# Kernel tuning notes

Hardware: AMD Instinct MI355X
Metric: run time of the kernel (lower is better)

## Reference

```python
import jax, jax.numpy as jnp
import numpy as np
from jax import lax

B, T, D, FF, E, TOPK, CLS = 16, 512, 1024, 2048, 4, 2, 1200
KW = 3  # conv kernel width per ff_kernelsize=[3,3]


def _sinusoidal_pe(T, D):
    pos = np.arange(T, dtype=np.float32)[:, None]
    div = np.exp(np.arange(0, D, 2, dtype=np.float32) * (-np.log(10000.0) / D))
    pe = np.zeros((T, D), dtype=np.float32)
    pe[:, 0::2] = np.sin(pos * div)
    pe[:, 1::2] = np.cos(pos * div)
    return jnp.asarray(pe)


def setup_inputs() -> dict:
    key = jax.random.key(0)
    ks = jax.random.split(key, 12)
    sc = 0.02
    x = jax.random.normal(ks[0], (B, T, D), jnp.float32)
    mask = jax.random.randint(ks[1], (B, T), 0, 2).astype(jnp.int32)
    mask = mask.at[:, 0].set(1)  # ensure >=1 valid token
    return {
        "x": x,
        "mask": mask,
        "fc1_w": jax.random.normal(ks[2], (D, D), jnp.float32) * sc,
        "fc1_b": jnp.zeros((D,), jnp.float32),
        "bn_g": jnp.ones((D,), jnp.float32),
        "bn_b": jnp.zeros((D,), jnp.float32),
        "pe": _sinusoidal_pe(T, D),
        "gate_w": jax.random.normal(ks[3], (D, E), jnp.float32) * sc,
        "ew1": jax.random.normal(ks[4], (E, FF, D, KW), jnp.float32) * sc,  # OIH per expert
        "eb1": jnp.zeros((E, FF), jnp.float32),
        "ew2": jax.random.normal(ks[5], (E, D, FF, KW), jnp.float32) * sc,
        "eb2": jnp.zeros((E, D), jnp.float32),
        "ln_g": jnp.ones((D,), jnp.float32),
        "ln_b": jnp.zeros((D,), jnp.float32),
        "out_w": jax.random.normal(ks[6], (CLS, D), jnp.float32) * sc,
        "out_b": jnp.zeros((CLS,), jnp.float32),
    }


def _forward(x, mask, fc1_w, fc1_b, bn_g, bn_b, pe, gate_w, ew1, eb1, ew2, eb2, ln_g, ln_b, out_w, out_b):
    mf = mask.astype(x.dtype)[..., None]  # [B,T,1]

    # fc1
    h = jnp.einsum("btd,ed->bte", x, fc1_w) + fc1_b

    # MaskedNorm (batch): stats over valid tokens only, invalid positions passed through
    cnt = jnp.maximum(jnp.sum(mf), 1.0)
    mean = jnp.sum(h * mf, axis=(0, 1)) / cnt
    var = jnp.sum(mf * (h - mean) ** 2, axis=(0, 1)) / cnt
    normed = (h - mean) * lax.rsqrt(var + 1e-5) * bn_g + bn_b
    h = jnp.where(mf > 0, normed, h)

    # ReLU + positional encoding (+ dropout is identity in eval)
    h = jax.nn.relu(h) + pe[None, :, :]

    # --- MoE with top-2 gating over 4 conv-FFN experts ---
    logits_g = jnp.einsum("btd,de->bte", h, gate_w)  # [B,T,E]
    probs_g = jax.nn.softmax(logits_g, axis=-1)
    top_v, top_i = lax.top_k(logits_g, TOPK)  # [B,T,K]
    top_g = jax.nn.softmax(top_v, axis=-1)
    # scatter top-k gates into dense [B,T,E] (E=4, cheap)
    gates = jnp.sum(top_g[..., None] * jax.nn.one_hot(top_i, E, dtype=h.dtype), axis=2)

    ht = jnp.transpose(h, (0, 2, 1))  # [B,D,T] for NCH conv

    def expert(w1, b1, w2, b2):
        y = lax.conv_general_dilated(ht, w1, (1,), "SAME", dimension_numbers=("NCH", "OIH", "NCH"))
        y = jax.nn.relu(y + b1[None, :, None])
        y = lax.conv_general_dilated(y, w2, (1,), "SAME", dimension_numbers=("NCH", "OIH", "NCH"))
        return y + b2[None, :, None]  # [B,D,T]

    ys = jax.vmap(expert)(ew1, eb1, ew2, eb2)  # [E,B,D,T]
    moe_out = jnp.einsum("bte,ebdt->btd", gates, ys)

    # load-balancing aux loss (Switch-style)
    frac = jnp.mean((gates > 0).astype(h.dtype), axis=(0, 1))  # tokens per expert
    imp = jnp.mean(probs_g, axis=(0, 1))
    aux_loss = E * jnp.sum(frac * imp)

    # LayerNorm (eps 1e-6)
    mu = jnp.mean(moe_out, axis=-1, keepdims=True)
    v = jnp.mean((moe_out - mu) ** 2, axis=-1, keepdims=True)
    feat = (moe_out - mu) * lax.rsqrt(v + 1e-6) * ln_g + ln_b

    logits = jnp.einsum("btd,cd->btc", feat, out_w) + out_b
    logp = jax.nn.log_softmax(logits, axis=2)
    p = jnp.exp(logp)
    feat_norm = feat / jnp.maximum(jnp.linalg.norm(feat, axis=-1, keepdims=True), 1e-12)
    return feat, feat_norm, logits, logp, p, aux_loss


def reference(x, mask, fc1_w, fc1_b, bn_g, bn_b, pe, gate_w, ew1, eb1, ew2, eb2, ln_g, ln_b, out_w, out_b):
    return _forward(x, mask, fc1_w, fc1_b, bn_g, bn_b, pe, gate_w, ew1, eb1, ew2, eb2, ln_g, ln_b, out_w, out_b)
```

## Files before the change

kernel.cpp:

```cpp
#include <hip/hip_runtime.h>
#include <hip/hip_bf16.h>


namespace {

constexpr int kB = 16, kT = 512, kD = 1024, kFF = 2048, kE = 4, kCLS = 1200;
constexpr int kM = kB * kT;
constexpr int kTP = kT + 2;
constexpr int kCLSP = 1280;
constexpr size_t kBTD = (size_t)kM * kD;
constexpr size_t kBTC = (size_t)kM * kCLS;
constexpr size_t kY1S = (size_t)kB * kTP * kFF;
constexpr size_t kTapStride = (size_t)kFF * kD;

constexpr size_t WS_H     = 0;
constexpr size_t WS_HPAD  = WS_H + kBTD;
constexpr size_t WS_Y1P   = WS_HPAD + (size_t)kB * kTP * kD / 2;
constexpr size_t WS_W1T   = WS_Y1P + (size_t)kB * kTP * kFF / 2;
constexpr size_t WS_W2T   = WS_W1T + (size_t)3 * kFF * kD / 2;
constexpr size_t WS_GATES = WS_W2T + (size_t)3 * kD * kFF / 2;
constexpr size_t WS_PROBS = WS_GATES + (size_t)kM * kE;
constexpr size_t WS_W1HI  = WS_PROBS + (size_t)kM * kE;
constexpr size_t WS_W1LO  = WS_W1HI + (size_t)kD * kD / 2;
constexpr size_t WS_OWB   = WS_W1LO + (size_t)kD * kD / 2;
constexpr size_t WS_SUMS  = WS_OWB + (size_t)kCLSP * kD / 2;
constexpr size_t WS_SUMSQ = WS_SUMS + kD;
constexpr size_t WS_CNT   = WS_SUMSQ + kD;
constexpr size_t WS_AA    = WS_CNT + 1;
constexpr size_t WS_CC    = WS_AA + kD;
constexpr int WS_ZERON = (int)(2 * kD + 1);

constexpr size_t BW_H     = 0;
constexpr size_t BW_HPAD  = BW_H + kBTD;
constexpr size_t BW_Y1    = BW_HPAD + (size_t)kB * kTP * kD / 2;
constexpr size_t BW_W1T   = BW_Y1 + (size_t)kE * kY1S / 2;
constexpr size_t BW_W2T   = BW_W1T + (size_t)kE * 3 * kFF * kD / 2;
constexpr size_t BW_GATES = BW_W2T + (size_t)kE * 3 * kD * kFF / 2;
constexpr size_t BW_PROBS = BW_GATES + (size_t)kM * kE;
constexpr size_t BW_W1HI  = BW_PROBS + (size_t)kM * kE;
constexpr size_t BW_W1LO  = BW_W1HI + (size_t)kD * kD / 2;
constexpr size_t BW_OWB   = BW_W1LO + (size_t)kD * kD / 2;
constexpr size_t BW_SUMS  = BW_OWB + (size_t)kCLSP * kD / 2;
constexpr size_t BW_SUMSQ = BW_SUMS + kD;
constexpr size_t BW_CNT   = BW_SUMSQ + kD;
constexpr size_t BW_AA    = BW_CNT + 1;
constexpr size_t BW_CC    = BW_AA + kD;
constexpr size_t BW_END   = BW_CC + kD;

typedef __attribute__((ext_vector_type(8))) short short8;
typedef __attribute__((ext_vector_type(4))) float f32x4;

#define GLOBAL_LOAD_LDS16(gp, lp)                                          \
  __builtin_amdgcn_global_load_lds(                                        \
      (const __attribute__((address_space(1))) void*)(gp),                 \
      (__attribute__((address_space(3))) void*)(lp), 16, 0, 0)

__device__ __forceinline__ float block_reduce_sum(float v, float* red) {
  const int tid = threadIdx.x;
  __syncthreads();
  red[tid] = v;
  __syncthreads();
  for (int s = 128; s > 0; s >>= 1) {
    if (tid < s) red[tid] += red[tid + s];
    __syncthreads();
  }
  return red[0];
}

__device__ __forceinline__ float block_reduce_max(float v, float* red) {
  const int tid = threadIdx.x;
  __syncthreads();
  red[tid] = v;
  __syncthreads();
  for (int s = 128; s > 0; s >>= 1) {
    if (tid < s) red[tid] = fmaxf(red[tid], red[tid + s]);
    __syncthreads();
  }
  return red[0];
}

__global__ void k_zero(float* __restrict__ p, int n) {
  int i = blockIdx.x * 256 + threadIdx.x;
  if (i < n) p[i] = 0.f;
}

__global__ void k_zero_bnd(__hip_bfloat16* __restrict__ Hpad,
                           __hip_bfloat16* __restrict__ Y1pad) {
  const int b = blockIdx.x >> 1;
  const int row = b * kTP + ((blockIdx.x & 1) ? (kTP - 1) : 0);
  const __hip_bfloat16 z = __float2bfloat16(0.f);
  for (int d = threadIdx.x; d < kD; d += 256) Hpad[(size_t)row * kD + d] = z;
  for (int d = threadIdx.x; d < kFF; d += 256) Y1pad[(size_t)row * kFF + d] = z;
}

__global__ void k_zero_bnd_all(__hip_bfloat16* __restrict__ Hpad,
                               __hip_bfloat16* __restrict__ Y1all) {
  const int g = blockIdx.x;
  const int which = g / (2 * kB);
  const int r = g % (2 * kB);
  const int b = r >> 1;
  const int row = b * kTP + ((r & 1) ? (kTP - 1) : 0);
  const __hip_bfloat16 z = __float2bfloat16(0.f);
  if (which == 0) {
    for (int d = threadIdx.x; d < kD; d += 256) Hpad[(size_t)row * kD + d] = z;
  } else {
    __hip_bfloat16* Y = Y1all + (size_t)(which - 1) * kY1S;
    for (int d = threadIdx.x; d < kFF; d += 256) Y[(size_t)row * kFF + d] = z;
  }
}

__global__ __launch_bounds__(256) void k_split(const float* __restrict__ src,
                                               __hip_bfloat16* __restrict__ hi,
                                               __hip_bfloat16* __restrict__ lo,
                                               int n4) {
  const int i = blockIdx.x * 256 + threadIdx.x;
  if (i >= n4) return;
  const float4 v = *reinterpret_cast<const float4*>(src + (size_t)i * 4);
  const float vv[4] = {v.x, v.y, v.z, v.w};
  unsigned short h[4], l[4];
#pragma unroll
  for (int j = 0; j < 4; ++j) {
    __hip_bfloat16 hb = __float2bfloat16(vv[j]);
    __hip_bfloat16 lb = __float2bfloat16(vv[j] - __bfloat162float(hb));
    h[j] = *reinterpret_cast<unsigned short*>(&hb);
    l[j] = *reinterpret_cast<unsigned short*>(&lb);
  }
  *reinterpret_cast<short4*>(hi + (size_t)i * 4) =
      make_short4(h[0], h[1], h[2], h[3]);
  *reinterpret_cast<short4*>(lo + (size_t)i * 4) =
      make_short4(l[0], l[1], l[2], l[3]);
}

__global__ __launch_bounds__(256) void k_wcast_pad(
    const float* __restrict__ w, __hip_bfloat16* __restrict__ dst) {
  const size_t i = (size_t)blockIdx.x * 256 + threadIdx.x;
  if (i >= (size_t)kCLSP * kD) return;
  const size_t r = i / kD;
  dst[i] = __float2bfloat16(r < kCLS ? w[i] : 0.f);
}

__global__ __launch_bounds__(256) void k_wt(const float* __restrict__ src,
                                            __hip_bfloat16* __restrict__ dst,
                                            int n) {
  const int i = blockIdx.x * 256 + threadIdx.x;
  if (i >= n) return;
  const float* s = src + (size_t)i * 3;
  dst[i] = __float2bfloat16(s[0]);
  dst[(size_t)n + i] = __float2bfloat16(s[1]);
  dst[(size_t)2 * n + i] = __float2bfloat16(s[2]);
}

__global__ __launch_bounds__(256) void k_wt_all(const float* __restrict__ ew1,
                                                const float* __restrict__ ew2,
                                                __hip_bfloat16* __restrict__ W1T,
                                                __hip_bfloat16* __restrict__ W2T) {
  const size_t n = (size_t)kFF * kD;
  const size_t total = (size_t)kE * n;
  const size_t i = (size_t)blockIdx.x * 256 + threadIdx.x;
  if (i >= total) return;
  const size_t e = i / n, j = i - e * n;
  {
    const float* s = ew1 + (e * n + j) * 3;
    __hip_bfloat16* d = W1T + e * 3 * n;
    d[j] = __float2bfloat16(s[0]);
    d[n + j] = __float2bfloat16(s[1]);
    d[2 * n + j] = __float2bfloat16(s[2]);
  }
  {
    const float* s = ew2 + (e * n + j) * 3;
    __hip_bfloat16* d = W2T + e * 3 * n;
    d[j] = __float2bfloat16(s[0]);
    d[n + j] = __float2bfloat16(s[1]);
    d[2 * n + j] = __float2bfloat16(s[2]);
  }
}

__global__ __launch_bounds__(256) void k_fc1_mfma(
    const __hip_bfloat16* __restrict__ Xhi, const __hip_bfloat16* __restrict__ Xlo,
    const __hip_bfloat16* __restrict__ Whi, const __hip_bfloat16* __restrict__ Wlo,
    const float* __restrict__ bias, float* __restrict__ H) {
  __shared__ __align__(16) __hip_bfloat16 As[128 * 32];
  __shared__ __align__(16) __hip_bfloat16 Bs[128 * 32];
  const int tid = threadIdx.x;
  const int m0 = blockIdx.y * 128;
  const int n0 = blockIdx.x * 128;
  const int w = tid >> 6, lane = tid & 63;
  const int wm = (w >> 1) * 64, wn = (w & 1) * 64;
  f32x4 acc[4][4] = {};
  const int fr = lane & 15, fc = (lane >> 4) * 8;
  const __hip_bfloat16* Aps[3] = {Xhi, Xlo, Xhi};
  const __hip_bfloat16* Bps[3] = {Whi, Whi, Wlo};
  for (int p = 0; p < 3; ++p) {
    const __hip_bfloat16* Ab = Aps[p] + (size_t)m0 * kD;
    const __hip_bfloat16* Bb = Bps[p] + (size_t)n0 * kD;
    for (int k0 = 0; k0 < kD; k0 += 32) {
      __syncthreads();
#pragma unroll
      for (int r = 0; r < 2; ++r) {
        const int idx = r * 256 + tid;
        const int row = idx >> 2, cg = (idx & 3) * 8;
        GLOBAL_LOAD_LDS16(Ab + (size_t)row * kD + k0 + cg, &As[idx * 8]);
        GLOBAL_LOAD_LDS16(Bb + (size_t)row * kD + k0 + cg, &Bs[idx * 8]);
      }
      __syncthreads();
      short8 af[4], bf[4];
#pragma unroll
      for (int i = 0; i < 4; ++i) {
        af[i] = *reinterpret_cast<const short8*>(&As[(wm + i * 16 + fr) * 32 + fc]);
        bf[i] = *reinterpret_cast<const short8*>(&Bs[(wn + i * 16 + fr) * 32 + fc]);
      }
#pragma unroll
      for (int i = 0; i < 4; ++i)
#pragma unroll
        for (int j = 0; j < 4; ++j)
          acc[i][j] = __builtin_amdgcn_mfma_f32_16x16x32_bf16(af[i], bf[j], acc[i][j], 0, 0, 0);
    }
  }
  const int cr = (lane >> 4) * 4, cc = lane & 15;
#pragma unroll
  for (int i = 0; i < 4; ++i) {
#pragma unroll
    for (int r = 0; r < 4; ++r) {
      const int m = m0 + wm + i * 16 + cr + r;
#pragma unroll
      for (int j = 0; j < 4; ++j) {
        const int gc = n0 + wn + j * 16 + cc;
        H[(size_t)m * kD + gc] = acc[i][j][r] + bias[gc];
      }
    }
  }
}

__global__ __launch_bounds__(256) void k_cls_mfma(
    const __hip_bfloat16* __restrict__ Fb, const __hip_bfloat16* __restrict__ Wb,
    const float* __restrict__ bias, float* __restrict__ logits) {
  __shared__ __align__(16) __hip_bfloat16 As[128 * 32];
  __shared__ __align__(16) __hip_bfloat16 Bs[128 * 32];
  const int tid = threadIdx.x;
  const int m0 = blockIdx.y * 128;
  const int n0 = blockIdx.x * 128;
  const int w = tid >> 6, lane = tid & 63;
  const int wm = (w >> 1) * 64, wn = (w & 1) * 64;
  f32x4 acc[4][4] = {};
  const int fr = lane & 15, fc = (lane >> 4) * 8;
  const __hip_bfloat16* Ab = Fb + (size_t)m0 * kD;
  const __hip_bfloat16* Bb = Wb + (size_t)n0 * kD;
  for (int k0 = 0; k0 < kD; k0 += 32) {
    __syncthreads();
#pragma unroll
    for (int r = 0; r < 2; ++r) {
      const int idx = r * 256 + tid;
      const int row = idx >> 2, cg = (idx & 3) * 8;
      GLOBAL_LOAD_LDS16(Ab + (size_t)row * kD + k0 + cg, &As[idx * 8]);
      GLOBAL_LOAD_LDS16(Bb + (size_t)row * kD + k0 + cg, &Bs[idx * 8]);
    }
    __syncthreads();
    short8 af[4], bf[4];
#pragma unroll
    for (int i = 0; i < 4; ++i) {
      af[i] = *reinterpret_cast<const short8*>(&As[(wm + i * 16 + fr) * 32 + fc]);
      bf[i] = *reinterpret_cast<const short8*>(&Bs[(wn + i * 16 + fr) * 32 + fc]);
    }
#pragma unroll
    for (int i = 0; i < 4; ++i)
#pragma unroll
      for (int j = 0; j < 4; ++j)
        acc[i][j] = __builtin_amdgcn_mfma_f32_16x16x32_bf16(af[i], bf[j], acc[i][j], 0, 0, 0);
  }
  const int cr = (lane >> 4) * 4, cc = lane & 15;
#pragma unroll
  for (int i = 0; i < 4; ++i) {
#pragma unroll
    for (int r = 0; r < 4; ++r) {
      const int m = m0 + wm + i * 16 + cr + r;
#pragma unroll
      for (int j = 0; j < 4; ++j) {
        const int gc = n0 + wn + j * 16 + cc;
        if (gc < kCLS) logits[(size_t)m * kCLS + gc] = acc[i][j][r] + bias[gc];
      }
    }
  }
}

__global__ __launch_bounds__(256) void k_conv1_mfma(
    const __hip_bfloat16* __restrict__ Hpad, const __hip_bfloat16* __restrict__ W1T,
    const float* __restrict__ b1, __hip_bfloat16* __restrict__ Y1pad) {
  __shared__ __align__(16) __hip_bfloat16 As[128 * 32];
  __shared__ __align__(16) __hip_bfloat16 Bs[128 * 32];
  const int tid = threadIdx.x;
  const int m0 = blockIdx.y * 128;
  const int n0 = blockIdx.x * 128;
  const int b = m0 >> 9;
  const int t0 = m0 & (kT - 1);
  const int arow0 = b * kTP + t0;
  const int w = tid >> 6, lane = tid & 63;
  const int wm = (w >> 1) * 64, wn = (w & 1) * 64;
  f32x4 acc[4][4] = {};
  const int fr = lane & 15, fc = (lane >> 4) * 8;
  for (int kk = 0; kk < 3; ++kk) {
    const __hip_bfloat16* Ab = Hpad + (size_t)(arow0 + kk) * kD;
    const __hip_bfloat16* Bb = W1T + (size_t)kk * kFF * kD + (size_t)n0 * kD;
    for (int k0 = 0; k0 < kD; k0 += 32) {
      __syncthreads();
#pragma unroll
      for (int r = 0; r < 2; ++r) {
        const int idx = r * 256 + tid;
        const int row = idx >> 2, cg = (idx & 3) * 8;
        GLOBAL_LOAD_LDS16(Ab + (size_t)row * kD + k0 + cg, &As[idx * 8]);
        GLOBAL_LOAD_LDS16(Bb + (size_t)row * kD + k0 + cg, &Bs[idx * 8]);
      }
      __syncthreads();
      short8 af[4], bf[4];
#pragma unroll
      for (int i = 0; i < 4; ++i) {
        af[i] = *reinterpret_cast<const short8*>(&As[(wm + i * 16 + fr) * 32 + fc]);
        bf[i] = *reinterpret_cast<const short8*>(&Bs[(wn + i * 16 + fr) * 32 + fc]);
      }
#pragma unroll
      for (int i = 0; i < 4; ++i)
#pragma unroll
        for (int j = 0; j < 4; ++j)
          acc[i][j] = __builtin_amdgcn_mfma_f32_16x16x32_bf16(af[i], bf[j], acc[i][j], 0, 0, 0);
    }
  }
  const int orow0 = b * kTP + t0 + 1;
  const int cr = (lane >> 4) * 4, cc = lane & 15;
#pragma unroll
  for (int i = 0; i < 4; ++i) {
#pragma unroll
    for (int r = 0; r < 4; ++r) {
      const int lr = wm + i * 16 + cr + r;
#pragma unroll
      for (int j = 0; j < 4; ++j) {
        const int gc = n0 + wn + j * 16 + cc;
        const float v = acc[i][j][r] + b1[gc];
        Y1pad[(size_t)(orow0 + lr) * kFF + gc] = __float2bfloat16(fmaxf(v, 0.f));
      }
    }
  }
}

__global__ __launch_bounds__(256) void k_conv2_mfma(
    const __hip_bfloat16* __restrict__ Y1pad, const __hip_bfloat16* __restrict__ W2T,
    const float* __restrict__ b2, const float* __restrict__ gates,
    int e, float* __restrict__ moe) {
  __shared__ __align__(16) __hip_bfloat16 As[128 * 32];
  __shared__ __align__(16) __hip_bfloat16 Bs[128 * 32];
  const int tid = threadIdx.x;
  const int m0 = blockIdx.y * 128;
  const int n0 = blockIdx.x * 128;
  const int b = m0 >> 9;
  const int t0 = m0 & (kT - 1);
  const int arow0 = b * kTP + t0;
  const int w = tid >> 6, lane = tid & 63;
  const int wm = (w >> 1) * 64, wn = (w & 1) * 64;
  f32x4 acc[4][4] = {};
  const int fr = lane & 15, fc = (lane >> 4) * 8;
  for (int kk = 0; kk < 3; ++kk) {
    const __hip_bfloat16* Ab = Y1pad + (size_t)(arow0 + kk) * kFF;
    const __hip_bfloat16* Bb = W2T + (size_t)kk * kD * kFF + (size_t)n0 * kFF;
    for (int k0 = 0; k0 < kFF; k0 += 32) {
      __syncthreads();
#pragma unroll
      for (int r = 0; r < 2; ++r) {
        const int idx = r * 256 + tid;
        const int row = idx >> 2, cg = (idx & 3) * 8;
        GLOBAL_LOAD_LDS16(Ab + (size_t)row * kFF + k0 + cg, &As[idx * 8]);
        GLOBAL_LOAD_LDS16(Bb + (size_t)row * kFF + k0 + cg, &Bs[idx * 8]);
      }
      __syncthreads();
      short8 af[4], bf[4];
#pragma unroll
      for (int i = 0; i < 4; ++i) {
        af[i] = *reinterpret_cast<const short8*>(&As[(wm + i * 16 + fr) * 32 + fc]);
        bf[i] = *reinterpret_cast<const short8*>(&Bs[(wn + i * 16 + fr) * 32 + fc]);
      }
#pragma unroll
      for (int i = 0; i < 4; ++i)
#pragma unroll
        for (int j = 0; j < 4; ++j)
          acc[i][j] = __builtin_amdgcn_mfma_f32_16x16x32_bf16(af[i], bf[j], acc[i][j], 0, 0, 0);
    }
  }
  const int cr = (lane >> 4) * 4, cc = lane & 15;
#pragma unroll
  for (int i = 0; i < 4; ++i) {
#pragma unroll
    for (int r = 0; r < 4; ++r) {
      const int lr = wm + i * 16 + cr + r;
      const int m = m0 + lr;
      const float g = gates[(size_t)m * kE + e];
#pragma unroll
      for (int j = 0; j < 4; ++j) {
        const int gc = n0 + wn + j * 16 + cc;
        const float v = acc[i][j][r] + b2[gc];
        const size_t idx = (size_t)m * kD + gc;
        moe[idx] = (e == 0 ? 0.f : moe[idx]) + g * v;
      }
    }
  }
}

#define WAITBAR(N)                                  \
  do {                                              \
    asm volatile("s_waitcnt vmcnt(" #N ")");        \
    __builtin_amdgcn_s_barrier();                   \
    __builtin_amdgcn_sched_barrier(0);              \
  } while (0)

#define QUAD(D, MH, NH, LOADA)                                                \
  do {                                                                        \
    const int _d = (D);                                                       \
    if (LOADA) {                                                              \
      const int _ab = ((_d * 2 + (MH)) << 14) + (fr << 6) + (fc << 1);        \
      _Pragma("unroll") for (int _i = 0; _i < 4; ++_i)                        \
          _Pragma("unroll") for (int _ks = 0; _ks < 2; ++_ks)                 \
              areg[_i][_ks] = *reinterpret_cast<const short8*>(               \
                  smem + ((_ab + (((wr * 4 + _i) * 2 + _ks) << 10)) ^ aswz)); \
    }                                                                         \
    short8 breg[2][2];                                                        \
    const int _bb =                                                           \
        65536 + ((_d * 2 + (NH)) << 14) + (fr << 6) + (fc << 1);              \
    _Pragma("unroll") for (int _j = 0; _j < 2; ++_j)                          \
        _Pragma("unroll") for (int _ks = 0; _ks < 2; ++_ks)                   \
            breg[_j][_ks] = *reinterpret_cast<const short8*>(                 \
                smem + ((_bb + (((wc * 2 + _j) * 2 + _ks) << 10)) ^ aswz));   \
    __builtin_amdgcn_s_setprio(1);                                            \
    _Pragma("unroll") for (int _i = 0; _i < 4; ++_i)                          \
        _Pragma("unroll") for (int _j = 0; _j < 2; ++_j)                      \
            _Pragma("unroll") for (int _ks = 0; _ks < 2; ++_ks)               \
                acc[MH][NH][_i][_j] =                                         \
                    __builtin_amdgcn_mfma_f32_16x16x32_bf16(                  \
                        areg[_i][_ks], breg[_j][_ks], acc[MH][NH][_i][_j],    \
                        0, 0, 0);                                             \
    __builtin_amdgcn_s_setprio(0);                                            \
  } while (0)

template <int K1, bool CONV1>
__global__ __launch_bounds__(512, 2) void k_conv8ph(
    const __hip_bfloat16* __restrict__ Asrc,
    const __hip_bfloat16* __restrict__ Wt,
    const float* __restrict__ bias,
    const float* __restrict__ gates,
    __hip_bfloat16* __restrict__ Yout,
    float* __restrict__ moe) {
  constexpr int NTOT = CONV1 ? kFF : kD;
  constexpr int NX = NTOT / 256;
  constexpr int NY = kM / 256;
  constexpr int NWG = kE * NY * NX;
  constexpr int KT1 = K1 / 64;
  constexpr int NT = 3 * KT1;
  extern __shared__ __align__(16) char smem[];

  int lid = blockIdx.x;
  lid = (lid & 7) * (NWG / 8) + (lid >> 3);
  const int e = lid / (NY * NX);
  const int rem = lid - e * (NY * NX);
  const int by = rem / NX, bx = rem - by * NX;
  const int m0 = by * 256, n0 = bx * 256;
  const int b = m0 >> 9, t0 = m0 & (kT - 1);
  const int arow0 = b * kTP + t0;

  const int tid = threadIdx.x;
  const int w = tid >> 6, l = tid & 63;
  const int wr = w >> 2, wc = w & 3;
  const int fr = l & 15, fc = (l >> 4) << 3;
  const int aswz = (fr & 8) ? 32 : 0;
  const int srr = l >> 2;
  const int scc = ((l & 3) << 3) ^ ((l & 32) ? 16 : 0);

  const __hip_bfloat16* Apan =
      (CONV1 ? Asrc : (Asrc + (size_t)e * kY1S)) + (size_t)arow0 * K1;
  const __hip_bfloat16* Bpan = Wt + (size_t)e * 3 * kTapStride + (size_t)n0 * K1;

  auto stageA = [&](int tau, int d, int mh) {
    const int kk = tau / KT1, kf = (tau % KT1) << 6;
    const __hip_bfloat16* org = Apan + (size_t)(kk + mh * 128) * K1 + kf;
    const int lb = (d * 2 + mh) << 14;
#pragma unroll
    for (int r = 0; r < 2; ++r) {
      const int s = w + r * 8;
      GLOBAL_LOAD_LDS16(org + (size_t)((s >> 1) * 16 + srr) * K1 +
                            ((s & 1) << 5) + scc,
                        smem + lb + (s << 10));
    }
  };
  auto stageB = [&](int tau, int d, int nh) {
    const int kk = tau / KT1, kf = (tau % KT1) << 6;
    const __hip_bfloat16* org =
        Bpan + (size_t)kk * kTapStride + (size_t)(nh * 128) * K1 + kf;
    const int lb = 65536 + ((d * 2 + nh) << 14);
#pragma unroll
    for (int r = 0; r < 2; ++r) {
      const int s = w + r * 8;
      GLOBAL_LOAD_LDS16(org + (size_t)((s >> 1) * 16 + srr) * K1 +
                            ((s & 1) << 5) + scc,
                        smem + lb + (s << 10));
    }
  };

  f32x4 acc[2][2][4][2] = {};
  short8 areg[4][2];

  stageA(0, 0, 0);
  stageB(0, 0, 0);
  stageB(0, 0, 1);
  stageA(0, 0, 1);

  for (int tau = 0; tau < NT - 1; ++tau) {
    const int d = tau & 1, dn = d ^ 1;
    WAITBAR(4); stageA(tau + 1, dn, 0); QUAD(d, 0, 0, true);
    WAITBAR(4); stageB(tau + 1, dn, 0); QUAD(d, 0, 1, false);
    WAITBAR(4); stageB(tau + 1, dn, 1); QUAD(d, 1, 0, true);
                stageA(tau + 1, dn, 1); QUAD(d, 1, 1, false);
  }
  {
    const int d = (NT - 1) & 1;
    WAITBAR(4); QUAD(d, 0, 0, true);
    WAITBAR(2); QUAD(d, 0, 1, false);
    WAITBAR(0); QUAD(d, 1, 0, true);
                QUAD(d, 1, 1, false);
  }

  const int cr = (l >> 4) * 4, cc = l & 15;
  if (CONV1) {
    __hip_bfloat16* Yb = Yout + (size_t)e * kY1S;
    const float* be = bias + (size_t)e * kFF;
    const int orow0 = b * kTP + t0 + 1;
#pragma unroll
    for (int mh = 0; mh < 2; ++mh)
#pragma unroll
      for (int i = 0; i < 4; ++i)
#pragma unroll
        for (int r = 0; r < 4; ++r) {
          const int rl = mh * 128 + wr * 64 + i * 16 + cr + r;
#pragma unroll
          for (int nh = 0; nh < 2; ++nh)
#pragma unroll
            for (int j = 0; j < 2; ++j) {
              const int gc = n0 + nh * 128 + wc * 32 + j * 16 + cc;
              const float v = acc[mh][nh][i][j][r] + be[gc];
              Yb[(size_t)(orow0 + rl) * kFF + gc] =
                  __float2bfloat16(fmaxf(v, 0.f));
            }
        }
  } else {
    const float* be = bias + (size_t)e * kD;
#pragma unroll
    for (int mh = 0; mh < 2; ++mh)
#pragma unroll
      for (int i = 0; i < 4; ++i)
#pragma unroll
        for (int r = 0; r < 4; ++r) {
          const int rl = mh * 128 + wr * 64 + i * 16 + cr + r;
          const int m = m0 + rl;
          const float g = gates[(size_t)m * kE + e];
#pragma unroll
          for (int nh = 0; nh < 2; ++nh)
#pragma unroll
            for (int j = 0; j < 2; ++j) {
              const int gc = n0 + nh * 128 + wc * 32 + j * 16 + cc;
              const float v = acc[mh][nh][i][j][r] + be[gc];
              atomicAdd(&moe[(size_t)m * kD + gc], g * v);
            }
        }
  }
}

__global__ __launch_bounds__(256) void k_cnt(const int* __restrict__ mask,
                                             float* __restrict__ cnt) {
  __shared__ float red[256];
  const int i = blockIdx.x * 256 + threadIdx.x;
  float v = (float)mask[i];
  v = block_reduce_sum(v, red);
  if (threadIdx.x == 0) atomicAdd(cnt, v);
}

__global__ __launch_bounds__(256) void k_stats(const float* __restrict__ H,
                                               const int* __restrict__ mask,
                                               float* __restrict__ sums,
                                               float* __restrict__ sumsq) {
  const int ch = blockIdx.x * 256 + threadIdx.x;
  const int r0 = blockIdx.y * 64;
  float s = 0.f, q = 0.f;
  for (int r = r0; r < r0 + 64; ++r) {
    if (mask[r]) {
      const float v = H[(size_t)r * kD + ch];
      s += v;
      q += v * v;
    }
  }
  atomicAdd(&sums[ch], s);
  atomicAdd(&sumsq[ch], q);
}

__global__ __launch_bounds__(256) void k_finalize(
    const float* __restrict__ sums, const float* __restrict__ sumsq,
    const float* __restrict__ cntp, const float* __restrict__ bn_g,
    const float* __restrict__ bn_b, float* __restrict__ aa,
    float* __restrict__ cc) {
  const int d = blockIdx.x * 256 + threadIdx.x;
  const float cnt = fmaxf(*cntp, 1.f);
  const float mean = sums[d] / cnt;
  const float var = sumsq[d] / cnt - mean * mean;
  const float istd = rsqrtf(var + 1e-5f);
  const float a = bn_g[d] * istd;
  aa[d] = a;
  cc[d] = bn_b[d] - mean * a;
}

__global__ __launch_bounds__(256) void k_norm_gate(
    const float* __restrict__ H, const int* __restrict__ mask,
    const float* __restrict__ pe, const float* __restrict__ aa,
    const float* __restrict__ cc, const float* __restrict__ gw,
    __hip_bfloat16* __restrict__ Hpad, float* __restrict__ gates,
    float* __restrict__ probs) {
  __shared__ float red[256];
  __shared__ float glog[4];
  const int r = blockIdx.x;
  const int tid = threadIdx.x;
  const int b = r >> 9;
  const int t = r & (kT - 1);
  const bool mv = mask[r] != 0;
  const size_t orow = (size_t)(b * kTP + t + 1) * kD;
  float gl[4] = {0.f, 0.f, 0.f, 0.f};
#pragma unroll
  for (int j = 0; j < 4; ++j) {
    const int d = tid + j * 256;
    float v = H[(size_t)r * kD + d];
    if (mv) v = v * aa[d] + cc[d];
    v = fmaxf(v, 0.f) + pe[(size_t)t * kD + d];
    Hpad[orow + d] = __float2bfloat16(v);
    const float4 g = *reinterpret_cast<const float4*>(gw + (size_t)d * 4);
    gl[0] += v * g.x; gl[1] += v * g.y; gl[2] += v * g.z; gl[3] += v * g.w;
  }
  for (int e = 0; e < 4; ++e) {
    const float s = block_reduce_sum(gl[e], red);
    if (tid == 0) glog[e] = s;
  }
  __syncthreads();
  if (tid == 0) {
    float lg[4] = {glog[0], glog[1], glog[2], glog[3]};
    const float mx = fmaxf(fmaxf(lg[0], lg[1]), fmaxf(lg[2], lg[3]));
    float ex[4], s = 0.f;
#pragma unroll
    for (int e = 0; e < 4; ++e) { ex[e] = expf(lg[e] - mx); s += ex[e]; }
    int i0 = 0;
    for (int e = 1; e < 4; ++e) if (lg[e] > lg[i0]) i0 = e;
    int i1 = -1;
    for (int e = 0; e < 4; ++e) {
      if (e == i0) continue;
      if (i1 < 0 || lg[e] > lg[i1]) i1 = e;
    }
    const float g0 = 1.f / (1.f + expf(lg[i1] - lg[i0]));
    float gv[4] = {0.f, 0.f, 0.f, 0.f};
    gv[i0] = g0;
    gv[i1] = 1.f - g0;
    *reinterpret_cast<float4*>(gates + (size_t)r * 4) =
        make_float4(gv[0], gv[1], gv[2], gv[3]);
    const float inv_s = 1.f / s;
    *reinterpret_cast<float4*>(probs + (size_t)r * 4) =
        make_float4(ex[0] * inv_s, ex[1] * inv_s, ex[2] * inv_s, ex[3] * inv_s);
  }
}

__global__ __launch_bounds__(256) void k_ln(
    const float* __restrict__ moe, const float* __restrict__ g,
    const float* __restrict__ b, float* __restrict__ feat,
    float* __restrict__ featn, __hip_bfloat16* __restrict__ featb) {
  __shared__ float red[256];
  const int r = blockIdx.x;
  const int tid = threadIdx.x;
  float v[4];
  float s = 0.f, q = 0.f;
#pragma unroll
  for (int j = 0; j < 4; ++j) {
    v[j] = moe[(size_t)r * kD + tid + j * 256];
    s += v[j];
    q += v[j] * v[j];
  }
  const float sum = block_reduce_sum(s, red);
  const float mu = sum * (1.f / kD);
  const float sq = block_reduce_sum(q, red);
  const float var = sq * (1.f / kD) - mu * mu;
  const float istd = rsqrtf(var + 1e-6f);
  float f[4];
  float fs = 0.f;
#pragma unroll
  for (int j = 0; j < 4; ++j) {
    const int d = tid + j * 256;
    f[j] = (v[j] - mu) * istd * g[d] + b[d];
    feat[(size_t)r * kD + d] = f[j];
    featb[(size_t)r * kD + d] = __float2bfloat16(f[j]);
    fs += f[j] * f[j];
  }
  const float nrm2 = block_reduce_sum(fs, red);
  const float scale = 1.f / fmaxf(sqrtf(nrm2), 1e-12f);
#pragma unroll
  for (int j = 0; j < 4; ++j) {
    const int d = tid + j * 256;
    featn[(size_t)r * kD + d] = f[j] * scale;
  }
}

__global__ __launch_bounds__(256) void k_softmax(
    const float* __restrict__ logits, float* __restrict__ logp,
    float* __restrict__ p) {
  __shared__ float red[256];
  const int r = blockIdx.x;
  const int tid = threadIdx.x;
  float lv[5];
  float mx = -1e30f;
#pragma unroll
  for (int j = 0; j < 5; ++j) {
    const int c = tid + j * 256;
    if (c < kCLS) {
      lv[j] = logits[(size_t)r * kCLS + c];
      mx = fmaxf(mx, lv[j]);
    }
  }
  mx = block_reduce_max(mx, red);
  float s = 0.f;
#pragma unroll
  for (int j = 0; j < 5; ++j) {
    const int c = tid + j * 256;
    if (c < kCLS) s += expf(lv[j] - mx);
  }
  s = block_reduce_sum(s, red);
  const float lse = mx + logf(s);
#pragma unroll
  for (int j = 0; j < 5; ++j) {
    const int c = tid + j * 256;
    if (c < kCLS) {
      const float lp = lv[j] - lse;
      logp[(size_t)r * kCLS + c] = lp;
      p[(size_t)r * kCLS + c] = expf(lp);
    }
  }
}

__global__ __launch_bounds__(256) void k_aux(const float* __restrict__ probs,
                                             const float* __restrict__ gates,
                                             float* __restrict__ out) {
  __shared__ float red[256];
  const int tid = threadIdx.x;
  float si[4] = {0.f, 0.f, 0.f, 0.f};
  float sf[4] = {0.f, 0.f, 0.f, 0.f};
  for (int i = tid; i < kM; i += 256) {
    const float4 p = *reinterpret_cast<const float4*>(probs + (size_t)i * 4);
    const float4 g = *reinterpret_cast<const float4*>(gates + (size_t)i * 4);
    si[0] += p.x; si[1] += p.y; si[2] += p.z; si[3] += p.w;
    sf[0] += (g.x > 0.f) ? 1.f : 0.f;
    sf[1] += (g.y > 0.f) ? 1.f : 0.f;
    sf[2] += (g.z > 0.f) ? 1.f : 0.f;
    sf[3] += (g.w > 0.f) ? 1.f : 0.f;
  }
  float tot = 0.f;
  for (int e = 0; e < 4; ++e) {
    const float S = block_reduce_sum(si[e], red);
    const float F = block_reduce_sum(sf[e], red);
    tot += (F / (float)kM) * (S / (float)kM);
  }
  if (tid == 0) out[0] = (float)kE * tot;
}

}

extern "C" void kernel_launch(void* const* d_in, const int* in_sizes, int n_in,
                              void* d_out, int out_size, void* d_ws,
                              size_t ws_size, hipStream_t stream) {
  const float* x     = (const float*)d_in[0];
  const int*   mask  = (const int*)d_in[1];
  const float* fc1_w = (const float*)d_in[2];
  const float* fc1_b = (const float*)d_in[3];
  const float* bn_g  = (const float*)d_in[4];
  const float* bn_b  = (const float*)d_in[5];
  const float* pe    = (const float*)d_in[6];
  const float* gw    = (const float*)d_in[7];
  const float* ew1   = (const float*)d_in[8];
  const float* eb1   = (const float*)d_in[9];
  const float* ew2   = (const float*)d_in[10];
  const float* eb2   = (const float*)d_in[11];
  const float* ln_g  = (const float*)d_in[12];
  const float* ln_b  = (const float*)d_in[13];
  const float* out_w = (const float*)d_in[14];
  const float* out_b = (const float*)d_in[15];

  float* ws = (float*)d_ws;

  float* outf   = (float*)d_out;
  float* feat   = outf;
  float* featn  = outf + kBTD;
  float* logits = outf + 2 * kBTD;
  float* logp   = logits + kBTC;
  float* pprob  = logp + kBTC;
  float* aux    = pprob + kBTC;

  const bool batched = ws_size >= BW_END * sizeof(float);

  if (batched) {
    float* H     = ws + BW_H;
    __hip_bfloat16* HPAD  = (__hip_bfloat16*)(ws + BW_HPAD);
    __hip_bfloat16* Y1ALL = (__hip_bfloat16*)(ws + BW_Y1);
    __hip_bfloat16* XHI   = Y1ALL;
    __hip_bfloat16* XLO   = XHI + kBTD;
    __hip_bfloat16* FEATB = Y1ALL;
    __hip_bfloat16* W1T   = (__hip_bfloat16*)(ws + BW_W1T);
    __hip_bfloat16* W2T   = (__hip_bfloat16*)(ws + BW_W2T);
    float* GATES = ws + BW_GATES;
    float* PROBS = ws + BW_PROBS;
    __hip_bfloat16* W1HI = (__hip_bfloat16*)(ws + BW_W1HI);
    __hip_bfloat16* W1LO = (__hip_bfloat16*)(ws + BW_W1LO);
    __hip_bfloat16* OWB  = (__hip_bfloat16*)(ws + BW_OWB);
    float* SUMS  = ws + BW_SUMS;
    float* MOE   = H;

    k_zero<<<dim3((WS_ZERON + 255) / 256), 256, 0, stream>>>(SUMS, WS_ZERON);
    k_split<<<dim3((int)(kBTD / 4 + 255) / 256), 256, 0, stream>>>(
        x, XHI, XLO, (int)(kBTD / 4));
    k_split<<<dim3((kD * kD / 4 + 255) / 256), 256, 0, stream>>>(
        fc1_w, W1HI, W1LO, kD * kD / 4);
    k_fc1_mfma<<<dim3(kD / 128, kM / 128), 256, 0, stream>>>(
        XHI, XLO, W1HI, W1LO, fc1_b, H);
    k_zero_bnd_all<<<dim3(2 * kB * (1 + kE)), 256, 0, stream>>>(HPAD, Y1ALL);
    k_wt_all<<<dim3((int)(((size_t)kE * kFF * kD + 255) / 256)), 256, 0,
               stream>>>(ew1, ew2, W1T, W2T);
    k_cnt<<<dim3(kM / 256), 256, 0, stream>>>(mask, ws + BW_CNT);
    k_stats<<<dim3(kD / 256, kM / 64), 256, 0, stream>>>(H, mask, SUMS,
                                                         ws + BW_SUMSQ);
    k_finalize<<<dim3(kD / 256), 256, 0, stream>>>(
        SUMS, ws + BW_SUMSQ, ws + BW_CNT, bn_g, bn_b, ws + BW_AA, ws + BW_CC);
    k_norm_gate<<<dim3(kM), 256, 0, stream>>>(H, mask, pe, ws + BW_AA,
                                              ws + BW_CC, gw, HPAD, GATES,
                                              PROBS);
    k_zero<<<dim3((int)((kBTD + 255) / 256)), 256, 0, stream>>>(MOE,
                                                                (int)kBTD);
    k_conv8ph<kD, true><<<dim3(kE * (kM / 256) * (kFF / 256)), 512, 131072,
                          stream>>>(HPAD, W1T, eb1, nullptr, Y1ALL, nullptr);
    k_conv8ph<kFF, false><<<dim3(kE * (kM / 256) * (kD / 256)), 512, 131072,
                            stream>>>(Y1ALL, W2T, eb2, GATES, nullptr, MOE);
    k_ln<<<dim3(kM), 256, 0, stream>>>(MOE, ln_g, ln_b, feat, featn, FEATB);
    k_wcast_pad<<<dim3((int)((size_t)kCLSP * kD + 255) / 256), 256, 0,
                  stream>>>(out_w, OWB);
    k_cls_mfma<<<dim3(kCLSP / 128, kM / 128), 256, 0, stream>>>(FEATB, OWB,
                                                                out_b, logits);
    k_softmax<<<dim3(kM), 256, 0, stream>>>(logits, logp, pprob);
    k_aux<<<1, 256, 0, stream>>>(PROBS, GATES, aux);
    return;
  }

  float* H     = ws + WS_H;
  __hip_bfloat16* HPAD  = (__hip_bfloat16*)(ws + WS_HPAD);
  __hip_bfloat16* Y1PAD = (__hip_bfloat16*)(ws + WS_Y1P);
  __hip_bfloat16* XHI   = (__hip_bfloat16*)(ws + WS_Y1P);
  __hip_bfloat16* XLO   = XHI + kBTD;
  __hip_bfloat16* FEATB = (__hip_bfloat16*)(ws + WS_Y1P);
  __hip_bfloat16* W1T   = (__hip_bfloat16*)(ws + WS_W1T);
  __hip_bfloat16* W2T   = (__hip_bfloat16*)(ws + WS_W2T);
  float* GATES = ws + WS_GATES;
  float* PROBS = ws + WS_PROBS;
  __hip_bfloat16* W1HI = (__hip_bfloat16*)(ws + WS_W1HI);
  __hip_bfloat16* W1LO = (__hip_bfloat16*)(ws + WS_W1LO);
  __hip_bfloat16* OWB  = (__hip_bfloat16*)(ws + WS_OWB);
  float* SUMS  = ws + WS_SUMS;
  float* SUMSQ = ws + WS_SUMSQ;
  float* CNT   = ws + WS_CNT;
  float* AA    = ws + WS_AA;
  float* CC    = ws + WS_CC;
  float* MOE   = H;

  k_zero<<<dim3((WS_ZERON + 255) / 256), 256, 0, stream>>>(SUMS, WS_ZERON);
  k_split<<<dim3((int)(kBTD / 4 + 255) / 256), 256, 0, stream>>>(x, XHI, XLO,
                                                                 (int)(kBTD / 4));
  k_split<<<dim3((kD * kD / 4 + 255) / 256), 256, 0, stream>>>(
      fc1_w, W1HI, W1LO, kD * kD / 4);
  k_fc1_mfma<<<dim3(kD / 128, kM / 128), 256, 0, stream>>>(XHI, XLO, W1HI,
                                                           W1LO, fc1_b, H);
  k_zero_bnd<<<dim3(2 * kB), 256, 0, stream>>>(HPAD, Y1PAD);
  k_cnt<<<dim3(kM / 256), 256, 0, stream>>>(mask, CNT);
  k_stats<<<dim3(kD / 256, kM / 64), 256, 0, stream>>>(H, mask, SUMS, SUMSQ);
  k_finalize<<<dim3(kD / 256), 256, 0, stream>>>(SUMS, SUMSQ, CNT, bn_g, bn_b,
                                                 AA, CC);
  k_norm_gate<<<dim3(kM), 256, 0, stream>>>(H, mask, pe, AA, CC, gw, HPAD,
                                            GATES, PROBS);
  for (int e = 0; e < kE; ++e) {
    k_wt<<<dim3((kFF * kD + 255) / 256), 256, 0, stream>>>(
        ew1 + (size_t)e * kFF * kD * 3, W1T, kFF * kD);
    k_wt<<<dim3((kD * kFF + 255) / 256), 256, 0, stream>>>(
        ew2 + (size_t)e * kD * kFF * 3, W2T, kD * kFF);
    k_conv1_mfma<<<dim3(kFF / 128, kM / 128), 256, 0, stream>>>(
        HPAD, W1T, eb1 + (size_t)e * kFF, Y1PAD);
    k_conv2_mfma<<<dim3(kD / 128, kM / 128), 256, 0, stream>>>(
        Y1PAD, W2T, eb2 + (size_t)e * kD, GATES, e, MOE);
  }
  k_ln<<<dim3(kM), 256, 0, stream>>>(MOE, ln_g, ln_b, feat, featn, FEATB);
  k_wcast_pad<<<dim3((int)((size_t)kCLSP * kD + 255) / 256), 256, 0, stream>>>(
      out_w, OWB);
  k_cls_mfma<<<dim3(kCLSP / 128, kM / 128), 256, 0, stream>>>(FEATB, OWB,
                                                              out_b, logits);
  k_softmax<<<dim3(kM), 256, 0, stream>>>(logits, logp, pprob);
  k_aux<<<1, 256, 0, stream>>>(PROBS, GATES, aux);
}
```

Measured before the change: 1.369 ms.

## Gather routed tokens per expert so conv2 skips tokens with zero gate

A new kernel builds a compacted list of token indices for each expert whose gate is nonzero, using a prefix scan. The second conv GEMM is replaced by a gather-based version that loads A rows through this list and returns early for tiles past the expert's token count. With top-2 of 4 gating this should roughly halve conv2 work. The cost is indirect row addressing, a small extra launch, and less regular memory access on the gathered rows.

```diff
diff --git a/kernel.cpp b/kernel.cpp
--- a/kernel.cpp
+++ b/kernel.cpp
@@ -45,7 +45,9 @@
 constexpr size_t BW_CNT   = BW_SUMSQ + kD;
 constexpr size_t BW_AA    = BW_CNT + 1;
 constexpr size_t BW_CC    = BW_AA + kD;
-constexpr size_t BW_END   = BW_CC + kD;
+constexpr size_t BW_ECNT  = BW_CC + kD;
+constexpr size_t BW_ELIST = BW_ECNT + 4;
+constexpr size_t BW_END   = BW_ELIST + (size_t)kE * kM;
 
 typedef __attribute__((ext_vector_type(8))) short short8;
 typedef __attribute__((ext_vector_type(4))) float f32x4;
@@ -173,6 +175,36 @@
     d[n + j] = __float2bfloat16(s[1]);
     d[2 * n + j] = __float2bfloat16(s[2]);
   }
+}
+
+__global__ __launch_bounds__(256) void k_build_elist(
+    const float* __restrict__ gates, int* __restrict__ elist,
+    int* __restrict__ ecnt) {
+  __shared__ int red[256];
+  const int e = blockIdx.x;
+  const int tid = threadIdx.x;
+  const int base = tid * 32;
+  int cnt = 0;
+  for (int j = 0; j < 32; ++j)
+    if (gates[(size_t)(base + j) * 4 + e] > 0.f) ++cnt;
+  red[tid] = cnt;
+  __syncthreads();
+  for (int s = 1; s < 256; s <<= 1) {
+    const int v = (tid >= s) ? red[tid - s] : 0;
+    __syncthreads();
+    red[tid] += v;
+    __syncthreads();
+  }
+  const int total = red[255];
+  int pos = red[tid] - cnt;
+  int* dst = elist + (size_t)e * kM;
+  for (int j = 0; j < 32; ++j) {
+    const int tk = base + j;
+    if (gates[(size_t)tk * 4 + e] > 0.f) dst[pos++] = tk;
+  }
+  const int padded = (total + 255) & ~255;
+  for (int i = total + tid; i < padded; i += 256) dst[i] = 0;
+  if (tid == 0) ecnt[e] = total;
 }
 
 __global__ __launch_bounds__(256) void k_fc1_mfma(
@@ -567,6 +599,122 @@
   }
 }
 
+__global__ __launch_bounds__(512, 2) void k_conv2sp(
+    const __hip_bfloat16* __restrict__ Y1all,
+    const __hip_bfloat16* __restrict__ W2T,
+    const float* __restrict__ b2, const float* __restrict__ gates,
+    const int* __restrict__ elist, const int* __restrict__ ecnt,
+    float* __restrict__ moe) {
+  constexpr int K1 = kFF;
+  constexpr int NX = kD / 256;
+  constexpr int NY = kM / 256;
+  constexpr int NWG = kE * NY * NX;
+  constexpr int KT1 = K1 / 64;
+  constexpr int NT = 3 * KT1;
+  extern __shared__ __align__(16) char smem[];
+
+  int lid = blockIdx.x;
+  lid = (lid & 7) * (NWG / 8) + (lid >> 3);
+  const int e = lid / (NY * NX);
+  const int rem = lid - e * (NY * NX);
+  const int by = rem / NX, bx = rem - by * NX;
+  const int m0 = by * 256, n0 = bx * 256;
+  const int cnt_e = ecnt[e];
+  if (m0 >= cnt_e) return;
+
+  const int tid = threadIdx.x;
+  const int w = tid >> 6, l = tid & 63;
+  const int wr = w >> 2, wc = w & 3;
+  const int fr = l & 15, fc = (l >> 4) << 3;
+  const int aswz = (fr & 8) ? 32 : 0;
+  const int srr = l >> 2;
+  const int scc = ((l & 3) << 3) ^ ((l & 32) ? 16 : 0);
+
+  const int* el = elist + (size_t)e * kM + m0;
+  const __hip_bfloat16* Ye = Y1all + (size_t)e * kY1S;
+  const __hip_bfloat16* Bpan =
+      W2T + (size_t)e * 3 * kTapStride + (size_t)n0 * K1;
+
+  const int colbits = ((w & 1) << 5) + scc;
+  const int r0 = (w >> 1) * 16 + srr;
+  const int r1 = r0 + 64;
+  const __hip_bfloat16* aptr[2][2];
+#pragma unroll
+  for (int mh = 0; mh < 2; ++mh) {
+    const int tk0 = el[mh * 128 + r0];
+    const int tk1 = el[mh * 128 + r1];
+    aptr[mh][0] = Ye +
+        (size_t)((tk0 >> 9) * kTP + (tk0 & (kT - 1))) * K1 + colbits;
+    aptr[mh][1] = Ye +
+        (size_t)((tk1 >> 9) * kTP + (tk1 & (kT - 1))) * K1 + colbits;
+  }
+
+  auto stageA = [&](int tau, int d, int mh) {
+    const int lb = (d * 2 + mh) << 14;
+    GLOBAL_LOAD_LDS16(aptr[mh][0] + tau * 64, smem + lb + (w << 10));
+    GLOBAL_LOAD_LDS16(aptr[mh][1] + tau * 64, smem + lb + ((w + 8) << 10));
+  };
+  auto stageB = [&](int tau, int d, int nh) {
+    const int kk = tau / KT1, kf = (tau % KT1) << 6;
+    const __hip_bfloat16* org =
+        Bpan + (size_t)kk * kTapStride + (size_t)(nh * 128) * K1 + kf;
+    const int lb = 65536 + ((d * 2 + nh) << 14);
+#pragma unroll
+    for (int r = 0; r < 2; ++r) {
+      const int s = w + r * 8;
+      GLOBAL_LOAD_LDS16(org + (size_t)((s >> 1) * 16 + srr) * K1 +
+                            ((s & 1) << 5) + scc,
+                        smem + lb + (s << 10));
+    }
+  };
+
+  f32x4 acc[2][2][4][2] = {};
+  short8 areg[4][2];
+
+  stageA(0, 0, 0);
+  stageB(0, 0, 0);
+  stageB(0, 0, 1);
+  stageA(0, 0, 1);
+
+  for (int tau = 0; tau < NT - 1; ++tau) {
+    const int d = tau & 1, dn = d ^ 1;
+    WAITBAR(4); stageA(tau + 1, dn, 0); QUAD(d, 0, 0, true);
+    WAITBAR(4); stageB(tau + 1, dn, 0); QUAD(d, 0, 1, false);
+    WAITBAR(4); stageB(tau + 1, dn, 1); QUAD(d, 1, 0, true);
+                stageA(tau + 1, dn, 1); QUAD(d, 1, 1, false);
+  }
+  {
+    const int d = (NT - 1) & 1;
+    WAITBAR(4); QUAD(d, 0, 0, true);
+    WAITBAR(2); QUAD(d, 0, 1, false);
+    WAITBAR(0); QUAD(d, 1, 0, true);
+                QUAD(d, 1, 1, false);
+  }
+
+  const int cr = (l >> 4) * 4, cc = l & 15;
+  const float* be = b2 + (size_t)e * kD;
+#pragma unroll
+  for (int mh = 0; mh < 2; ++mh)
+#pragma unroll
+    for (int i = 0; i < 4; ++i)
+#pragma unroll
+      for (int r = 0; r < 4; ++r) {
+        const int rl = mh * 128 + wr * 64 + i * 16 + cr + r;
+        if (m0 + rl < cnt_e) {
+          const int tk = el[rl];
+          const float g = gates[(size_t)tk * 4 + e];
+#pragma unroll
+          for (int nh = 0; nh < 2; ++nh)
+#pragma unroll
+            for (int j = 0; j < 2; ++j) {
+              const int gc = n0 + nh * 128 + wc * 32 + j * 16 + cc;
+              const float v = acc[mh][nh][i][j][r] + be[gc];
+              atomicAdd(&moe[(size_t)tk * kD + gc], g * v);
+            }
+        }
+      }
+}
+
 __global__ __launch_bounds__(256) void k_cnt(const int* __restrict__ mask,
                                              float* __restrict__ cnt) {
   __shared__ float red[256];
@@ -813,6 +961,8 @@
     __hip_bfloat16* W1LO = (__hip_bfloat16*)(ws + BW_W1LO);
     __hip_bfloat16* OWB  = (__hip_bfloat16*)(ws + BW_OWB);
     float* SUMS  = ws + BW_SUMS;
+    int*   ECNT  = (int*)(ws + BW_ECNT);
+    int*   ELIST = (int*)(ws + BW_ELIST);
     float* MOE   = H;
 
     k_zero<<<dim3((WS_ZERON + 255) / 256), 256, 0, stream>>>(SUMS, WS_ZERON);
@@ -833,12 +983,13 @@
     k_norm_gate<<<dim3(kM), 256, 0, stream>>>(H, mask, pe, ws + BW_AA,
                                               ws + BW_CC, gw, HPAD, GATES,
                                               PROBS);
+    k_build_elist<<<dim3(kE), 256, 0, stream>>>(GATES, ELIST, ECNT);
     k_zero<<<dim3((int)((kBTD + 255) / 256)), 256, 0, stream>>>(MOE,
                                                                 (int)kBTD);
     k_conv8ph<kD, true><<<dim3(kE * (kM / 256) * (kFF / 256)), 512, 131072,
                           stream>>>(HPAD, W1T, eb1, nullptr, Y1ALL, nullptr);
-    k_conv8ph<kFF, false><<<dim3(kE * (kM / 256) * (kD / 256)), 512, 131072,
-                            stream>>>(Y1ALL, W2T, eb2, GATES, nullptr, MOE);
+    k_conv2sp<<<dim3(kE * (kM / 256) * (kD / 256)), 512, 131072, stream>>>(
+        Y1ALL, W2T, eb2, GATES, ELIST, ECNT, MOE);
     k_ln<<<dim3(kM), 256, 0, stream>>>(MOE, ln_g, ln_b, feat, featn, FEATB);
     k_wcast_pad<<<dim3((int)((size_t)kCLSP * kD + 255) / 256), 256, 0,
                   stream>>>(out_w, OWB);
```

Result: slower. 1.409 ms (+2.9%).
